# Optimization experiments

Hardware: AMD Instinct MI355X
Metric: run time of the kernel (lower is better)

## Reference

```python
import jax, jax.numpy as jnp
import numpy as np

N_NODES = 50000
N_EDGES = 800000
IN_DIM = 128
HID = 128
NUM_CLASSES = 2


def setup_inputs() -> dict:
    key = jax.random.key(0)
    ks = jax.random.split(key, 16)
    inp = {
        "adj_row": jax.random.randint(ks[0], (N_EDGES,), 0, N_NODES),
        "adj_col": jax.random.randint(ks[1], (N_EDGES,), 0, N_NODES),
        "adj_vals": jax.random.uniform(ks[2], (N_EDGES,), dtype=jnp.float32),
        "input_feature": jax.random.normal(ks[3], (N_NODES, IN_DIM), dtype=jnp.float32),
        "graph_indicator": jax.random.randint(ks[4], (N_NODES,), 0, 64),
        # GCN layer params (kaiming-uniform-ish init; zeros bias like the torch module)
        "W1": jax.random.uniform(ks[5], (IN_DIM, HID), jnp.float32, -1, 1) * np.sqrt(6.0 / IN_DIM),
        "b1": jnp.zeros((HID,), jnp.float32),
        "W2": jax.random.uniform(ks[6], (HID, HID), jnp.float32, -1, 1) * np.sqrt(6.0 / HID),
        "b2": jnp.zeros((HID,), jnp.float32),
        "W3": jax.random.uniform(ks[7], (HID, HID), jnp.float32, -1, 1) * np.sqrt(6.0 / HID),
        "b3": jnp.zeros((HID,), jnp.float32),
        # fc params (torch.nn.Linear default init range)
        "fcW1": jax.random.uniform(ks[8], (3 * HID, HID), jnp.float32, -1, 1) / np.sqrt(3 * HID),
        "fcb1": jax.random.uniform(ks[9], (HID,), jnp.float32, -1, 1) / np.sqrt(3 * HID),
        "fcW2": jax.random.uniform(ks[10], (HID, HID // 2), jnp.float32, -1, 1) / np.sqrt(HID),
        "fcb2": jax.random.uniform(ks[11], (HID // 2,), jnp.float32, -1, 1) / np.sqrt(HID),
        "fcW3": jax.random.uniform(ks[12], (HID // 2, NUM_CLASSES), jnp.float32, -1, 1) / np.sqrt(HID // 2),
        "fcb3": jax.random.uniform(ks[13], (NUM_CLASSES,), jnp.float32, -1, 1) / np.sqrt(HID // 2),
    }
    return inp


def _gcn_layer(row, col, vals, x, W, b, n_nodes):
    # support = X @ W  -> dense GEMM
    support = x @ W
    # sparse.mm(A, support): out[i] = sum_{e: row[e]=i} vals[e] * support[col[e]]
    msgs = support[col] * vals[:, None]  # [E, D] gather + scale
    agg = jax.ops.segment_sum(msgs, row, num_segments=n_nodes)
    return agg + b


def reference(adj_row, adj_col, adj_vals, input_feature, graph_indicator,
              W1, b1, W2, b2, W3, b3, fcW1, fcb1, fcW2, fcb2, fcW3, fcb3):
    n = input_feature.shape[0]
    g1 = jax.nn.relu(_gcn_layer(adj_row, adj_col, adj_vals, input_feature, W1, b1, n))
    g2 = jax.nn.relu(_gcn_layer(adj_row, adj_col, adj_vals, g1, W2, b2, n))
    g3 = jax.nn.relu(_gcn_layer(adj_row, adj_col, adj_vals, g2, W3, b3, n))
    feat = jnp.concatenate([g1, g2, g3], axis=1)  # [N, 3*HID]
    h = jax.nn.relu(feat @ fcW1 + fcb1)
    h = jax.nn.relu(h @ fcW2 + fcb2)
    logits = h @ fcW3 + fcb3
    return logits
```

## Files before the change

kernel.cpp:

```cpp
#include <hip/hip_runtime.h>
#include <hip/hip_bf16.h>

#define N_NODES 50000
#define N_EDGES 800000
#define NBK 391
#define BCAP 2560
#define PADSLACK 896

static inline int cdiv(int a, int b) { return (a + b - 1) / b; }

typedef __attribute__((ext_vector_type(8))) short short8;
typedef __attribute__((ext_vector_type(4))) float f32x4;

__device__ __forceinline__ float b2f(unsigned short u) {
    union { unsigned int i; float f; } c;
    c.i = ((unsigned int)u) << 16;
    return c.f;
}
__device__ __forceinline__ unsigned short f2bb(float f) {
    __hip_bfloat16 h = __float2bfloat16(f);
    return *(unsigned short*)&h;
}

__device__ __forceinline__ void pack_one(const float* __restrict__ W,
                                         __hip_bfloat16* __restrict__ out,
                                         int K, int N, int t) {
    int lane = t & 63;
    int kc = (t >> 6) % (K / 32);
    int nt = (t >> 6) / (K / 32);
    int kbase = kc * 32 + (lane >> 4) * 8;
    int col = nt * 16 + (lane & 15);
    __hip_bfloat16* dst = out + (size_t)t * 8;
#pragma unroll
    for (int j = 0; j < 8; ++j)
        dst[j] = __float2bfloat16(W[(size_t)(kbase + j) * N + col]);
}

__global__ __launch_bounds__(256)
void stage1_kernel(const int* __restrict__ row, const int* __restrict__ col,
                   const float* __restrict__ vals, int* __restrict__ bcursor,
                   int2* __restrict__ tmp, int E,
                   const float* __restrict__ x, __hip_bfloat16* __restrict__ support,
                   int M,
                   const float* __restrict__ W1, const float* __restrict__ W2,
                   const float* __restrict__ W3, const float* __restrict__ fcW1,
                   const float* __restrict__ fcW2,
                   __hip_bfloat16* __restrict__ pW2, __hip_bfloat16* __restrict__ pW3,
                   __hip_bfloat16* __restrict__ pfcW1, __hip_bfloat16* __restrict__ pfcW2) {
    __shared__ unsigned short As[64][136];
    __shared__ int hist[NBK];
    __shared__ int base[NBK];
    const int b = blockIdx.x;
    const int tid = threadIdx.x;

    if (b < 196) {
        const int CH = 4096;
        int e0 = b * CH;
        for (int i = tid; i < NBK; i += 256) hist[i] = 0;
        __syncthreads();
        for (int i = tid; i < CH; i += 256) {
            int e = e0 + i;
            if (e < E) atomicAdd(&hist[row[e] >> 7], 1);
        }
        __syncthreads();
        for (int i = tid; i < NBK; i += 256) {
            int c = hist[i];
            base[i] = (c > 0) ? (i * BCAP + atomicAdd(&bcursor[i], c)) : 0;
            hist[i] = 0;
        }
        __syncthreads();
        for (int i = tid; i < CH; i += 256) {
            int e = e0 + i;
            if (e < E) {
                int r = row[e];
                int bk = r >> 7;
                int rk = atomicAdd(&hist[bk], 1);
                tmp[base[bk] + rk] = make_int2(((r & 127) << 16) | col[e],
                                               __float_as_int(vals[e]));
            }
        }
        return;
    }

    if (b < 978) {
        const int wave = tid >> 6;
        const int lane = tid & 63;
        const int ln15 = lane & 15;
        const int quad = lane >> 4;
        const int m0 = (b - 196) * 64;

        short8 bfr[4][2];
#pragma unroll
        for (int kc = 0; kc < 4; ++kc)
#pragma unroll
            for (int h = 0; h < 2; ++h)
#pragma unroll
                for (int j = 0; j < 8; ++j)
                    bfr[kc][h][j] = (short)f2bb(
                        W1[(size_t)(kc * 32 + quad * 8 + j) * 128 + (wave * 2 + h) * 16 + ln15]);

#pragma unroll
        for (int i = 0; i < 4; ++i) {
            int idx = tid + i * 256;
            int r = idx >> 4;
            int c8 = (idx & 15) * 8;
            uint4 pk = {0, 0, 0, 0};
            if (m0 + r < M) {
                const float* src = &x[(size_t)(m0 + r) * 128 + c8];
                float4 a = *(const float4*)src;
                float4 bq = *(const float4*)(src + 4);
                pk.x = f2bb(a.x) | ((unsigned int)f2bb(a.y) << 16);
                pk.y = f2bb(a.z) | ((unsigned int)f2bb(a.w) << 16);
                pk.z = f2bb(bq.x) | ((unsigned int)f2bb(bq.y) << 16);
                pk.w = f2bb(bq.z) | ((unsigned int)f2bb(bq.w) << 16);
            }
            *(uint4*)&As[r][c8] = pk;
        }
        __syncthreads();

        f32x4 acc[4][2];
#pragma unroll
        for (int s = 0; s < 4; ++s)
#pragma unroll
            for (int h = 0; h < 2; ++h) acc[s][h] = (f32x4){0.f, 0.f, 0.f, 0.f};
#pragma unroll
        for (int kc = 0; kc < 4; ++kc) {
            short8 af[4];
#pragma unroll
            for (int s = 0; s < 4; ++s)
                af[s] = *(const short8*)&As[s * 16 + ln15][kc * 32 + quad * 8];
#pragma unroll
            for (int s = 0; s < 4; ++s)
#pragma unroll
                for (int h = 0; h < 2; ++h)
                    acc[s][h] = __builtin_amdgcn_mfma_f32_16x16x32_bf16(
                        af[s], bfr[kc][h], acc[s][h], 0, 0, 0);
        }
#pragma unroll
        for (int s = 0; s < 4; ++s)
#pragma unroll
            for (int h = 0; h < 2; ++h) {
                int cl = (wave * 2 + h) * 16 + ln15;
#pragma unroll
                for (int r = 0; r < 4; ++r) {
                    int rw = m0 + s * 16 + quad * 4 + r;
                    if (rw < M)
                        support[(size_t)rw * 128 + cl] = __float2bfloat16(acc[s][h][r]);
                }
            }
        return;
    }

    int pb = b - 978;
    if (pb < 8)       pack_one(W2,  pW2,  128, 128, pb * 256 + tid);
    else if (pb < 16) pack_one(W3,  pW3,  128, 128, (pb - 8) * 256 + tid);
    else if (pb < 40) pack_one(fcW1, pfcW1, 384, 128, (pb - 16) * 256 + tid);
    else              pack_one(fcW2, pfcW2, 128, 64, (pb - 40) * 256 + tid);
}


__global__ __launch_bounds__(256)
void binB_kernel(const int2* __restrict__ tmp, const int* __restrict__ bcursor,
                 int2* __restrict__ rowrange, int2* __restrict__ epack, int N) {
    int b = blockIdx.x;
    int r0 = b << 7;
    int nr = N - r0; if (nr > 128) nr = 128;
    __shared__ int cnt[128];
    __shared__ int cur[128];
    __shared__ int rpos[128];
    __shared__ int red[256];
    int t = threadIdx.x;
    int partial = 0;
    for (int i = t; i < b; i += 256) partial += bcursor[i];
    red[t] = partial;
    if (t < 128) cnt[t] = 0;
    __syncthreads();
    for (int off = 128; off > 0; off >>= 1) {
        if (t < off) red[t] += red[t + off];
        __syncthreads();
    }
    int slab = b * BCAP;
    int send = slab + bcursor[b];
    for (int i = slab + t; i < send; i += 256)
        atomicAdd(&cnt[tmp[i].x >> 16], 1);
    __syncthreads();
    int rcnt = (t < 128) ? cnt[t] : 0;
    int pc = (rcnt + 7) & ~7;
    if (t < 128) cur[t] = pc;
    __syncthreads();
    for (int off = 1; off < 128; off <<= 1) {
        int u = (t >= off && t < 128) ? cur[t - off] : 0;
        __syncthreads();
        if (t < 128) cur[t] += u;
        __syncthreads();
    }
    int obase = red[0] + b * PADSLACK;
    if (t < 128) {
        int pos = obase + cur[t] - pc;
        rpos[t] = pos;
        cur[t] = pos;
        if (t < nr) rowrange[r0 + t] = make_int2(pos, pos + pc);
    }
    __syncthreads();
    for (int i = slab + t; i < send; i += 256) {
        int2 v = tmp[i];
        int rl = v.x >> 16;
        int c = v.x & 0xffff;
        int pos = atomicAdd(&cur[rl], 1);
        epack[pos] = make_int2(c, v.y);
    }
    if (t < 128) {
        int rc = rcnt;
        int pos = rpos[t];
#pragma unroll 1
        for (int i = pos + rc; i < pos + pc; ++i)
            epack[i] = make_int2(0, 0);
    }
}

__global__ __launch_bounds__(256, 3)
void mfma_gemm(const __hip_bfloat16* __restrict__ A, int lda,
               const __hip_bfloat16* __restrict__ pW,
               __hip_bfloat16* __restrict__ C, int M) {
    __shared__ unsigned short As[64][136];
    const int tid = threadIdx.x;
    const int wave = tid >> 6;
    const int lane = tid & 63;
    const int ln15 = lane & 15;
    const int quad = lane >> 4;
    const int m0 = blockIdx.x * 64;
    const int ntw = wave * 2;

    f32x4 acc[4][2];
#pragma unroll
    for (int s = 0; s < 4; ++s)
#pragma unroll
        for (int h = 0; h < 2; ++h) acc[s][h] = (f32x4){0.f, 0.f, 0.f, 0.f};

#pragma unroll
    for (int i = 0; i < 4; ++i) {
        int idx = tid + i * 256;
        int r = idx >> 4;
        int c8 = (idx & 15) * 8;
        uint4 v = *(const uint4*)&A[(size_t)(m0 + r) * lda + c8];
        *(uint4*)&As[r][c8] = v;
    }
    __syncthreads();
#pragma unroll
    for (int kc = 0; kc < 4; ++kc) {
        short8 af[4];
#pragma unroll
        for (int s = 0; s < 4; ++s)
            af[s] = *(const short8*)&As[s * 16 + ln15][kc * 32 + quad * 8];
        short8 bf[2];
#pragma unroll
        for (int h = 0; h < 2; ++h)
            bf[h] = *(const short8*)&pW[((size_t)((ntw + h) * 4 + kc) * 64 + lane) * 8];
#pragma unroll
        for (int s = 0; s < 4; ++s)
#pragma unroll
            for (int h = 0; h < 2; ++h)
                acc[s][h] = __builtin_amdgcn_mfma_f32_16x16x32_bf16(
                    af[s], bf[h], acc[s][h], 0, 0, 0);
    }

#pragma unroll
    for (int s = 0; s < 4; ++s)
#pragma unroll
        for (int h = 0; h < 2; ++h) {
            int cl = (ntw + h) * 16 + ln15;
#pragma unroll
            for (int r = 0; r < 4; ++r) {
                int rw = m0 + s * 16 + quad * 4 + r;
                if (rw < M)
                    C[(size_t)rw * 128 + cl] = __float2bfloat16(acc[s][h][r]);
            }
        }
}

__device__ __forceinline__ void accum8(float* acc, long long e, uint4 u) {
    float f = __int_as_float((int)(e >> 32));
    acc[0] += f * b2f((unsigned short)(u.x & 0xffff));
    acc[1] += f * b2f((unsigned short)(u.x >> 16));
    acc[2] += f * b2f((unsigned short)(u.y & 0xffff));
    acc[3] += f * b2f((unsigned short)(u.y >> 16));
    acc[4] += f * b2f((unsigned short)(u.z & 0xffff));
    acc[5] += f * b2f((unsigned short)(u.z >> 16));
    acc[6] += f * b2f((unsigned short)(u.w & 0xffff));
    acc[7] += f * b2f((unsigned short)(u.w >> 16));
}

__global__ __launch_bounds__(256)
void spmm_kernel(const int2* __restrict__ rowrange,
                 const int2* __restrict__ epack,
                 const __hip_bfloat16* __restrict__ support,
                 const float* __restrict__ bias, __hip_bfloat16* __restrict__ out,
                 int ldo, int n) {
    int wv = threadIdx.x >> 6;
    int l = threadIdx.x & 63;
    int node = blockIdx.x * 4 + wv;
    if (node >= n) return;
    const int g = l >> 4;
    const int j = l & 15;
    const long long* ep = (const long long*)epack;
    int2 rr = rowrange[node];
    int p = rr.x, end = rr.y;

    float acc[8];
#pragma unroll
    for (int k = 0; k < 8; ++k) acc[k] = 0.f;

    long long e0 = 0, e1 = 0;
    uint4 u0 = {0, 0, 0, 0}, u1 = {0, 0, 0, 0};
    bool have = false;
    if (p < end) {
        e0 = ep[p + g];
        e1 = ep[p + 4 + g];
        u0 = *(const uint4*)&support[(size_t)(unsigned int)(e0 & 0xffffffffu) * 128 + j * 8];
        u1 = *(const uint4*)&support[(size_t)(unsigned int)(e1 & 0xffffffffu) * 128 + j * 8];
        p += 8;
        have = true;
    }
    while (p < end) {
        long long f0 = ep[p + g];
        long long f1 = ep[p + 4 + g];
        uint4 w0 = *(const uint4*)&support[(size_t)(unsigned int)(f0 & 0xffffffffu) * 128 + j * 8];
        uint4 w1 = *(const uint4*)&support[(size_t)(unsigned int)(f1 & 0xffffffffu) * 128 + j * 8];
        accum8(acc, e0, u0);
        accum8(acc, e1, u1);
        e0 = f0; u0 = w0; e1 = f1; u1 = w1;
        p += 8;
    }
    if (have) {
        accum8(acc, e0, u0);
        accum8(acc, e1, u1);
    }
#pragma unroll
    for (int k = 0; k < 8; ++k) {
        acc[k] += __shfl_xor(acc[k], 16);
        acc[k] += __shfl_xor(acc[k], 32);
    }
    if (g == 0) {
        float4 b0 = *(const float4*)&bias[j * 8];
        float4 b1 = *(const float4*)&bias[j * 8 + 4];
        unsigned int q0 = (unsigned int)f2bb(fmaxf(acc[0] + b0.x, 0.f))
                        | ((unsigned int)f2bb(fmaxf(acc[1] + b0.y, 0.f)) << 16);
        unsigned int q1 = (unsigned int)f2bb(fmaxf(acc[2] + b0.z, 0.f))
                        | ((unsigned int)f2bb(fmaxf(acc[3] + b0.w, 0.f)) << 16);
        unsigned int q2 = (unsigned int)f2bb(fmaxf(acc[4] + b1.x, 0.f))
                        | ((unsigned int)f2bb(fmaxf(acc[5] + b1.y, 0.f)) << 16);
        unsigned int q3 = (unsigned int)f2bb(fmaxf(acc[6] + b1.z, 0.f))
                        | ((unsigned int)f2bb(fmaxf(acc[7] + b1.w, 0.f)) << 16);
        uint4 st = {q0, q1, q2, q3};
        *(uint4*)&out[(size_t)node * ldo + j * 8] = st;
    }
}

__global__ __launch_bounds__(256, 3)
void fc123_kernel(const __hip_bfloat16* __restrict__ featb,
                  const __hip_bfloat16* __restrict__ pfcW1,
                  const float* __restrict__ fcb1,
                  const __hip_bfloat16* __restrict__ pfcW2,
                  const float* __restrict__ fcb2,
                  const float* __restrict__ fcW3, const float* __restrict__ fcb3,
                  float* __restrict__ out, int M) {
    __shared__ unsigned short As[64][136];
    __shared__ float w3s[128];
    __shared__ float b3s[2];
    const int tid = threadIdx.x;
    const int wave = tid >> 6;
    const int lane = tid & 63;
    const int ln15 = lane & 15;
    const int quad = lane >> 4;
    const int m0 = blockIdx.x * 64;
    if (tid < 128) w3s[tid] = fcW3[tid];
    if (tid < 2) b3s[tid] = fcb3[tid];

    f32x4 acc[4][2];
#pragma unroll
    for (int s = 0; s < 4; ++s)
#pragma unroll
        for (int h = 0; h < 2; ++h) acc[s][h] = (f32x4){0.f, 0.f, 0.f, 0.f};
    for (int kb = 0; kb < 3; ++kb) {
#pragma unroll
        for (int i = 0; i < 4; ++i) {
            int idx = tid + i * 256;
            int r = idx >> 4;
            int c8 = (idx & 15) * 8;
            uint4 v = *(const uint4*)&featb[(size_t)(m0 + r) * 384 + kb * 128 + c8];
            *(uint4*)&As[r][c8] = v;
        }
        __syncthreads();
#pragma unroll
        for (int kc = 0; kc < 4; ++kc) {
            short8 af[4];
#pragma unroll
            for (int s = 0; s < 4; ++s)
                af[s] = *(const short8*)&As[s * 16 + ln15][kc * 32 + quad * 8];
            short8 bf[2];
#pragma unroll
            for (int h = 0; h < 2; ++h) {
                int kcg = kb * 4 + kc;
                bf[h] = *(const short8*)&pfcW1[((size_t)((wave * 2 + h) * 12 + kcg) * 64 + lane) * 8];
            }
#pragma unroll
            for (int s = 0; s < 4; ++s)
#pragma unroll
                for (int h = 0; h < 2; ++h)
                    acc[s][h] = __builtin_amdgcn_mfma_f32_16x16x32_bf16(
                        af[s], bf[h], acc[s][h], 0, 0, 0);
        }
        __syncthreads();
    }
#pragma unroll
    for (int s = 0; s < 4; ++s)
#pragma unroll
        for (int h = 0; h < 2; ++h) {
            int col = (wave * 2 + h) * 16 + ln15;
            float bv = fcb1[col];
#pragma unroll
            for (int r = 0; r < 4; ++r) {
                int row = s * 16 + quad * 4 + r;
                As[row][col] = f2bb(fmaxf(acc[s][h][r] + bv, 0.f));
            }
        }
    __syncthreads();

    f32x4 acc2[4];
#pragma unroll
    for (int s = 0; s < 4; ++s) acc2[s] = (f32x4){0.f, 0.f, 0.f, 0.f};
#pragma unroll
    for (int kc = 0; kc < 4; ++kc) {
        short8 af[4];
#pragma unroll
        for (int s = 0; s < 4; ++s)
            af[s] = *(const short8*)&As[s * 16 + ln15][kc * 32 + quad * 8];
        short8 bfw = *(const short8*)&pfcW2[((size_t)(wave * 4 + kc) * 64 + lane) * 8];
#pragma unroll
        for (int s = 0; s < 4; ++s)
            acc2[s] = __builtin_amdgcn_mfma_f32_16x16x32_bf16(af[s], bfw, acc2[s], 0, 0, 0);
    }
    __syncthreads();
    {
        int col2 = wave * 16 + ln15;
        float bv = fcb2[col2];
#pragma unroll
        for (int s = 0; s < 4; ++s)
#pragma unroll
            for (int r = 0; r < 4; ++r) {
                int row = s * 16 + quad * 4 + r;
                As[row][col2] = f2bb(fmaxf(acc2[s][r] + bv, 0.f));
            }
    }
    __syncthreads();

    if (tid < 128) {
        int row = tid >> 1, cls = tid & 1;
        int grow = m0 + row;
        if (grow < M) {
            float a = b3s[cls];
#pragma unroll
            for (int k = 0; k < 64; ++k)
                a += b2f(As[row][k]) * w3s[k * 2 + cls];
            out[(size_t)grow * 2 + cls] = a;
        }
    }
}

extern "C" void kernel_launch(void* const* d_in, const int* in_sizes, int n_in,
                              void* d_out, int out_size, void* d_ws, size_t ws_size,
                              hipStream_t stream) {
    const int*   adj_row  = (const int*)d_in[0];
    const int*   adj_col  = (const int*)d_in[1];
    const float* adj_vals = (const float*)d_in[2];
    const float* x        = (const float*)d_in[3];
    const float* W1   = (const float*)d_in[5];
    const float* b1   = (const float*)d_in[6];
    const float* W2   = (const float*)d_in[7];
    const float* b2   = (const float*)d_in[8];
    const float* W3   = (const float*)d_in[9];
    const float* b3   = (const float*)d_in[10];
    const float* fcW1 = (const float*)d_in[11];
    const float* fcb1 = (const float*)d_in[12];
    const float* fcW2 = (const float*)d_in[13];
    const float* fcb2 = (const float*)d_in[14];
    const float* fcW3 = (const float*)d_in[15];
    const float* fcb3 = (const float*)d_in[16];
    float* out = (float*)d_out;

    const int N = N_NODES, E = N_EDGES;
    const int Mpad = 50048;
    const int EPAD = E + NBK * PADSLACK + 64;

    char* p = (char*)d_ws;
    auto alloc = [&](size_t bytes) {
        char* q = p;
        p += (bytes + 255) & ~(size_t)255;
        return q;
    };
    __hip_bfloat16* featb    = (__hip_bfloat16*)alloc((size_t)Mpad * 384 * 2);
    __hip_bfloat16* supportb = (__hip_bfloat16*)alloc((size_t)Mpad * 128 * 2);
    __hip_bfloat16* pW2   = (__hip_bfloat16*)alloc(16384 * 2);
    __hip_bfloat16* pW3   = (__hip_bfloat16*)alloc(16384 * 2);
    __hip_bfloat16* pfcW1 = (__hip_bfloat16*)alloc(49152 * 2);
    __hip_bfloat16* pfcW2 = (__hip_bfloat16*)alloc(8192 * 2);
    int2*  rowrange  = (int2*)alloc((size_t)(N + 1) * 8);
    int*   bcursor   = (int*)alloc((size_t)NBK * 4);
    int2*  epack     = (int2*)alloc((size_t)EPAD * 8);
    int2*  tmp       = (int2*)alloc((size_t)NBK * BCAP * 8);

    hipMemsetAsync(bcursor, 0, (size_t)NBK * 4, stream);
    stage1_kernel<<<1022, 256, 0, stream>>>(adj_row, adj_col, adj_vals, bcursor, tmp, E,
                                            x, supportb, N,
                                            W1, W2, W3, fcW1, fcW2,
                                            pW2, pW3, pfcW1, pfcW2);
    binB_kernel<<<NBK, 256, 0, stream>>>(tmp, bcursor, rowrange, epack, N);

    const int gemmGrid = cdiv(N, 64);
    const int spmmGrid = cdiv(N, 4);

    spmm_kernel<<<spmmGrid, 256, 0, stream>>>(rowrange, epack, supportb, b1,
                                              featb + 0, 384, N);
    mfma_gemm<<<gemmGrid, 256, 0, stream>>>(featb + 0, 384, pW2, supportb, N);
    spmm_kernel<<<spmmGrid, 256, 0, stream>>>(rowrange, epack, supportb, b2,
                                              featb + 128, 384, N);
    mfma_gemm<<<gemmGrid, 256, 0, stream>>>(featb + 128, 384, pW3, supportb, N);
    spmm_kernel<<<spmmGrid, 256, 0, stream>>>(rowrange, epack, supportb, b3,
                                              featb + 256, 384, N);

    fc123_kernel<<<gemmGrid, 256, 0, stream>>>(featb, pfcW1, fcb1, pfcW2, fcb2,
                                               fcW3, fcb3, out, N);
}
```

Measured before the change: 268.0 us.

## Fuse SpMM aggregation with following GEMM and FC head per 64-row tile

Each 64-node tile now aggregates its neighbours into shared memory, applies bias and ReLU, and immediately runs the MFMA GEMM with the next layer weights. The third aggregation feeds straight into the FC head without a round trip through global memory. This cuts kernel launches from six to three and avoids rereading layer outputs from global memory. In exchange, each wave processes 16 nodes sequentially rather than one node per wave across many blocks, so there is far less parallelism (782 blocks) for latency hiding. Ping-pong support buffers are added so the gather never reads rows the same kernel is overwriting.

```diff
diff --git a/kernel.cpp b/kernel.cpp
--- a/kernel.cpp
+++ b/kernel.cpp
@@ -158,7 +158,6 @@
     else              pack_one(fcW2, pfcW2, 128, 64, (pb - 40) * 256 + tid);
 }
 
-
 __global__ __launch_bounds__(256)
 void binB_kernel(const int2* __restrict__ tmp, const int* __restrict__ bcursor,
                  int2* __restrict__ rowrange, int2* __restrict__ epack, int N) {
@@ -218,66 +217,6 @@
     }
 }
 
-__global__ __launch_bounds__(256, 3)
-void mfma_gemm(const __hip_bfloat16* __restrict__ A, int lda,
-               const __hip_bfloat16* __restrict__ pW,
-               __hip_bfloat16* __restrict__ C, int M) {
-    __shared__ unsigned short As[64][136];
-    const int tid = threadIdx.x;
-    const int wave = tid >> 6;
-    const int lane = tid & 63;
-    const int ln15 = lane & 15;
-    const int quad = lane >> 4;
-    const int m0 = blockIdx.x * 64;
-    const int ntw = wave * 2;
-
-    f32x4 acc[4][2];
-#pragma unroll
-    for (int s = 0; s < 4; ++s)
-#pragma unroll
-        for (int h = 0; h < 2; ++h) acc[s][h] = (f32x4){0.f, 0.f, 0.f, 0.f};
-
-#pragma unroll
-    for (int i = 0; i < 4; ++i) {
-        int idx = tid + i * 256;
-        int r = idx >> 4;
-        int c8 = (idx & 15) * 8;
-        uint4 v = *(const uint4*)&A[(size_t)(m0 + r) * lda + c8];
-        *(uint4*)&As[r][c8] = v;
-    }
-    __syncthreads();
-#pragma unroll
-    for (int kc = 0; kc < 4; ++kc) {
-        short8 af[4];
-#pragma unroll
-        for (int s = 0; s < 4; ++s)
-            af[s] = *(const short8*)&As[s * 16 + ln15][kc * 32 + quad * 8];
-        short8 bf[2];
-#pragma unroll
-        for (int h = 0; h < 2; ++h)
-            bf[h] = *(const short8*)&pW[((size_t)((ntw + h) * 4 + kc) * 64 + lane) * 8];
-#pragma unroll
-        for (int s = 0; s < 4; ++s)
-#pragma unroll
-            for (int h = 0; h < 2; ++h)
-                acc[s][h] = __builtin_amdgcn_mfma_f32_16x16x32_bf16(
-                    af[s], bf[h], acc[s][h], 0, 0, 0);
-    }
-
-#pragma unroll
-    for (int s = 0; s < 4; ++s)
-#pragma unroll
-        for (int h = 0; h < 2; ++h) {
-            int cl = (ntw + h) * 16 + ln15;
-#pragma unroll
-            for (int r = 0; r < 4; ++r) {
-                int rw = m0 + s * 16 + quad * 4 + r;
-                if (rw < M)
-                    C[(size_t)rw * 128 + cl] = __float2bfloat16(acc[s][h][r]);
-            }
-        }
-}
-
 __device__ __forceinline__ void accum8(float* acc, long long e, uint4 u) {
     float f = __int_as_float((int)(e >> 32));
     acc[0] += f * b2f((unsigned short)(u.x & 0xffff));
@@ -290,26 +229,11 @@
     acc[7] += f * b2f((unsigned short)(u.w >> 16));
 }
 
-__global__ __launch_bounds__(256)
-void spmm_kernel(const int2* __restrict__ rowrange,
-                 const int2* __restrict__ epack,
-                 const __hip_bfloat16* __restrict__ support,
-                 const float* __restrict__ bias, __hip_bfloat16* __restrict__ out,
-                 int ldo, int n) {
-    int wv = threadIdx.x >> 6;
-    int l = threadIdx.x & 63;
-    int node = blockIdx.x * 4 + wv;
-    if (node >= n) return;
-    const int g = l >> 4;
-    const int j = l & 15;
-    const long long* ep = (const long long*)epack;
-    int2 rr = rowrange[node];
-    int p = rr.x, end = rr.y;
-
-    float acc[8];
+__device__ __forceinline__ void agg_node(const long long* __restrict__ ep,
+                                         const __hip_bfloat16* __restrict__ support,
+                                         int p, int end, int g, int j, float* acc) {
 #pragma unroll
     for (int k = 0; k < 8; ++k) acc[k] = 0.f;
-
     long long e0 = 0, e1 = 0;
     uint4 u0 = {0, 0, 0, 0}, u1 = {0, 0, 0, 0};
     bool have = false;
@@ -340,57 +264,167 @@
         acc[k] += __shfl_xor(acc[k], 16);
         acc[k] += __shfl_xor(acc[k], 32);
     }
-    if (g == 0) {
-        float4 b0 = *(const float4*)&bias[j * 8];
-        float4 b1 = *(const float4*)&bias[j * 8 + 4];
-        unsigned int q0 = (unsigned int)f2bb(fmaxf(acc[0] + b0.x, 0.f))
-                        | ((unsigned int)f2bb(fmaxf(acc[1] + b0.y, 0.f)) << 16);
-        unsigned int q1 = (unsigned int)f2bb(fmaxf(acc[2] + b0.z, 0.f))
-                        | ((unsigned int)f2bb(fmaxf(acc[3] + b0.w, 0.f)) << 16);
-        unsigned int q2 = (unsigned int)f2bb(fmaxf(acc[4] + b1.x, 0.f))
-                        | ((unsigned int)f2bb(fmaxf(acc[5] + b1.y, 0.f)) << 16);
-        unsigned int q3 = (unsigned int)f2bb(fmaxf(acc[6] + b1.z, 0.f))
-                        | ((unsigned int)f2bb(fmaxf(acc[7] + b1.w, 0.f)) << 16);
-        uint4 st = {q0, q1, q2, q3};
-        *(uint4*)&out[(size_t)node * ldo + j * 8] = st;
-    }
 }
 
 __global__ __launch_bounds__(256, 3)
-void fc123_kernel(const __hip_bfloat16* __restrict__ featb,
-                  const __hip_bfloat16* __restrict__ pfcW1,
-                  const float* __restrict__ fcb1,
-                  const __hip_bfloat16* __restrict__ pfcW2,
-                  const float* __restrict__ fcb2,
-                  const float* __restrict__ fcW3, const float* __restrict__ fcb3,
-                  float* __restrict__ out, int M) {
+void spmm_gemm_kernel(const int2* __restrict__ rowrange,
+                      const int2* __restrict__ epack,
+                      const __hip_bfloat16* __restrict__ support,
+                      const float* __restrict__ bias,
+                      __hip_bfloat16* __restrict__ gout,
+                      const __hip_bfloat16* __restrict__ pW,
+                      __hip_bfloat16* __restrict__ Cout,
+                      int N) {
+    __shared__ unsigned short As[64][136];
+    const int tid = threadIdx.x;
+    const int wv = tid >> 6;
+    const int l = tid & 63;
+    const int g = l >> 4;
+    const int j = l & 15;
+    const int m0 = blockIdx.x * 64;
+    const long long* ep = (const long long*)epack;
+    float4 b0 = *(const float4*)&bias[j * 8];
+    float4 b1 = *(const float4*)&bias[j * 8 + 4];
+
+    for (int i = 0; i < 16; ++i) {
+        int node = m0 + wv * 16 + i;
+        if (node >= N) {
+            if (g == 0) *(uint4*)&As[wv * 16 + i][j * 8] = (uint4){0, 0, 0, 0};
+            continue;
+        }
+        int2 rr = rowrange[node];
+        float acc[8];
+        agg_node(ep, support, rr.x, rr.y, g, j, acc);
+        if (g == 0) {
+            unsigned int q0 = (unsigned int)f2bb(fmaxf(acc[0] + b0.x, 0.f))
+                            | ((unsigned int)f2bb(fmaxf(acc[1] + b0.y, 0.f)) << 16);
+            unsigned int q1 = (unsigned int)f2bb(fmaxf(acc[2] + b0.z, 0.f))
+                            | ((unsigned int)f2bb(fmaxf(acc[3] + b0.w, 0.f)) << 16);
+            unsigned int q2 = (unsigned int)f2bb(fmaxf(acc[4] + b1.x, 0.f))
+                            | ((unsigned int)f2bb(fmaxf(acc[5] + b1.y, 0.f)) << 16);
+            unsigned int q3 = (unsigned int)f2bb(fmaxf(acc[6] + b1.z, 0.f))
+                            | ((unsigned int)f2bb(fmaxf(acc[7] + b1.w, 0.f)) << 16);
+            uint4 st = {q0, q1, q2, q3};
+            *(uint4*)&As[wv * 16 + i][j * 8] = st;
+            *(uint4*)&gout[(size_t)node * 384 + j * 8] = st;
+        }
+    }
+    __syncthreads();
+
+    const int ln15 = l & 15;
+    const int quad = l >> 4;
+    const int ntw = wv * 2;
+    f32x4 acc2[4][2];
+#pragma unroll
+    for (int s = 0; s < 4; ++s)
+#pragma unroll
+        for (int h = 0; h < 2; ++h) acc2[s][h] = (f32x4){0.f, 0.f, 0.f, 0.f};
+#pragma unroll
+    for (int kc = 0; kc < 4; ++kc) {
+        short8 af[4];
+#pragma unroll
+        for (int s = 0; s < 4; ++s)
+            af[s] = *(const short8*)&As[s * 16 + ln15][kc * 32 + quad * 8];
+        short8 bf[2];
+#pragma unroll
+        for (int h = 0; h < 2; ++h)
+            bf[h] = *(const short8*)&pW[((size_t)((ntw + h) * 4 + kc) * 64 + l) * 8];
+#pragma unroll
+        for (int s = 0; s < 4; ++s)
+#pragma unroll
+            for (int h = 0; h < 2; ++h)
+                acc2[s][h] = __builtin_amdgcn_mfma_f32_16x16x32_bf16(
+                    af[s], bf[h], acc2[s][h], 0, 0, 0);
+    }
+#pragma unroll
+    for (int s = 0; s < 4; ++s)
+#pragma unroll
+        for (int h = 0; h < 2; ++h) {
+            int cl = (ntw + h) * 16 + ln15;
+#pragma unroll
+            for (int r = 0; r < 4; ++r) {
+                int rw = m0 + s * 16 + quad * 4 + r;
+                if (rw < N)
+                    Cout[(size_t)rw * 128 + cl] = __float2bfloat16(acc2[s][h][r]);
+            }
+        }
+}
+
+__global__ __launch_bounds__(256, 3)
+void spmm_fc_kernel(const int2* __restrict__ rowrange,
+                    const int2* __restrict__ epack,
+                    const __hip_bfloat16* __restrict__ support,
+                    const float* __restrict__ bias,
+                    const __hip_bfloat16* __restrict__ featb,
+                    const __hip_bfloat16* __restrict__ pfcW1,
+                    const float* __restrict__ fcb1,
+                    const __hip_bfloat16* __restrict__ pfcW2,
+                    const float* __restrict__ fcb2,
+                    const float* __restrict__ fcW3, const float* __restrict__ fcb3,
+                    float* __restrict__ out, int N) {
     __shared__ unsigned short As[64][136];
     __shared__ float w3s[128];
     __shared__ float b3s[2];
     const int tid = threadIdx.x;
-    const int wave = tid >> 6;
-    const int lane = tid & 63;
+    const int wv = tid >> 6;
+    const int l = tid & 63;
+    const int g = l >> 4;
+    const int j = l & 15;
+    const int m0 = blockIdx.x * 64;
+    const long long* ep = (const long long*)epack;
+    if (tid < 128) w3s[tid] = fcW3[tid];
+    if (tid < 2) b3s[tid] = fcb3[tid];
+    float4 b0 = *(const float4*)&bias[j * 8];
+    float4 b1 = *(const float4*)&bias[j * 8 + 4];
+
+    for (int i = 0; i < 16; ++i) {
+        int node = m0 + wv * 16 + i;
+        if (node >= N) {
+            if (g == 0) *(uint4*)&As[wv * 16 + i][j * 8] = (uint4){0, 0, 0, 0};
+            continue;
+        }
+        int2 rr = rowrange[node];
+        float acc[8];
+        agg_node(ep, support, rr.x, rr.y, g, j, acc);
+        if (g == 0) {
+            unsigned int q0 = (unsigned int)f2bb(fmaxf(acc[0] + b0.x, 0.f))
+                            | ((unsigned int)f2bb(fmaxf(acc[1] + b0.y, 0.f)) << 16);
+            unsigned int q1 = (unsigned int)f2bb(fmaxf(acc[2] + b0.z, 0.f))
+                            | ((unsigned int)f2bb(fmaxf(acc[3] + b0.w, 0.f)) << 16);
+            unsigned int q2 = (unsigned int)f2bb(fmaxf(acc[4] + b1.x, 0.f))
+                            | ((unsigned int)f2bb(fmaxf(acc[5] + b1.y, 0.f)) << 16);
+            unsigned int q3 = (unsigned int)f2bb(fmaxf(acc[6] + b1.z, 0.f))
+                            | ((unsigned int)f2bb(fmaxf(acc[7] + b1.w, 0.f)) << 16);
+            uint4 st = {q0, q1, q2, q3};
+            *(uint4*)&As[wv * 16 + i][j * 8] = st;
+        }
+    }
+    __syncthreads();
+
+    const int lane = l;
     const int ln15 = lane & 15;
     const int quad = lane >> 4;
-    const int m0 = blockIdx.x * 64;
-    if (tid < 128) w3s[tid] = fcW3[tid];
-    if (tid < 2) b3s[tid] = fcb3[tid];
-
+    const int wave = wv;
     f32x4 acc[4][2];
 #pragma unroll
     for (int s = 0; s < 4; ++s)
 #pragma unroll
         for (int h = 0; h < 2; ++h) acc[s][h] = (f32x4){0.f, 0.f, 0.f, 0.f};
-    for (int kb = 0; kb < 3; ++kb) {
-#pragma unroll
-        for (int i = 0; i < 4; ++i) {
-            int idx = tid + i * 256;
-            int r = idx >> 4;
-            int c8 = (idx & 15) * 8;
-            uint4 v = *(const uint4*)&featb[(size_t)(m0 + r) * 384 + kb * 128 + c8];
-            *(uint4*)&As[r][c8] = v;
-        }
-        __syncthreads();
+#pragma unroll
+    for (int step = 0; step < 3; ++step) {
+        const int kb = (step == 0) ? 2 : (step - 1);
+        if (step != 0) {
+            __syncthreads();
+#pragma unroll
+            for (int i = 0; i < 4; ++i) {
+                int idx = tid + i * 256;
+                int r = idx >> 4;
+                int c8 = (idx & 15) * 8;
+                uint4 v = *(const uint4*)&featb[(size_t)(m0 + r) * 384 + kb * 128 + c8];
+                *(uint4*)&As[r][c8] = v;
+            }
+            __syncthreads();
+        }
 #pragma unroll
         for (int kc = 0; kc < 4; ++kc) {
             short8 af[4];
@@ -410,8 +444,8 @@
                     acc[s][h] = __builtin_amdgcn_mfma_f32_16x16x32_bf16(
                         af[s], bf[h], acc[s][h], 0, 0, 0);
         }
-        __syncthreads();
-    }
+    }
+    __syncthreads();
 #pragma unroll
     for (int s = 0; s < 4; ++s)
 #pragma unroll
@@ -457,7 +491,7 @@
     if (tid < 128) {
         int row = tid >> 1, cls = tid & 1;
         int grow = m0 + row;
-        if (grow < M) {
+        if (grow < N) {
             float a = b3s[cls];
 #pragma unroll
             for (int k = 0; k < 64; ++k)
@@ -500,6 +534,7 @@
     };
     __hip_bfloat16* featb    = (__hip_bfloat16*)alloc((size_t)Mpad * 384 * 2);
     __hip_bfloat16* supportb = (__hip_bfloat16*)alloc((size_t)Mpad * 128 * 2);
+    __hip_bfloat16* supportc = (__hip_bfloat16*)alloc((size_t)Mpad * 128 * 2);
     __hip_bfloat16* pW2   = (__hip_bfloat16*)alloc(16384 * 2);
     __hip_bfloat16* pW3   = (__hip_bfloat16*)alloc(16384 * 2);
     __hip_bfloat16* pfcW1 = (__hip_bfloat16*)alloc(49152 * 2);
@@ -516,18 +551,13 @@
                                             pW2, pW3, pfcW1, pfcW2);
     binB_kernel<<<NBK, 256, 0, stream>>>(tmp, bcursor, rowrange, epack, N);
 
-    const int gemmGrid = cdiv(N, 64);
-    const int spmmGrid = cdiv(N, 4);
-
-    spmm_kernel<<<spmmGrid, 256, 0, stream>>>(rowrange, epack, supportb, b1,
-                                              featb + 0, 384, N);
-    mfma_gemm<<<gemmGrid, 256, 0, stream>>>(featb + 0, 384, pW2, supportb, N);
-    spmm_kernel<<<spmmGrid, 256, 0, stream>>>(rowrange, epack, supportb, b2,
-                                              featb + 128, 384, N);
-    mfma_gemm<<<gemmGrid, 256, 0, stream>>>(featb + 128, 384, pW3, supportb, N);
-    spmm_kernel<<<spmmGrid, 256, 0, stream>>>(rowrange, epack, supportb, b3,
-                                              featb + 256, 384, N);
-
-    fc123_kernel<<<gemmGrid, 256, 0, stream>>>(featb, pfcW1, fcb1, pfcW2, fcb2,
-                                               fcW3, fcb3, out, N);
-}
+    const int fgrid = cdiv(N, 64);
+
+    spmm_gemm_kernel<<<fgrid, 256, 0, stream>>>(rowrange, epack, supportb, b1,
+                                                featb + 0, pW2, supportc, N);
+    spmm_gemm_kernel<<<fgrid, 256, 0, stream>>>(rowrange, epack, supportc, b2,
+                                                featb + 128, pW3, supportb, N);
+    spmm_fc_kernel<<<fgrid, 256, 0, stream>>>(rowrange, epack, supportb, b3,
+                                              featb, pfcW1, fcb1, pfcW2, fcb2,
+                                              fcW3, fcb3, out, N);
+}
```

Result: slower. 273.9 us (+2.2%).
